# Kernel optimization log

Measured on AMD Instinct MI355X. Metric: run time of the kernel, lower is better.

The kernel has to match this reference:

```python
import jax, jax.numpy as jnp
import numpy as np

STRIDES = (8, 16, 32)
FMP = ((160, 160), (80, 80), (40, 40))
NUM_CLASSES = 80
TOPK = 1000
CONF_THRESH = 0.05
NMS_THRESH = 0.6
IMG_MAX = 1280.0
CLASS_OFFSET = 8192.0  # > any box coordinate, separates classes for batched NMS


def setup_inputs() -> dict:
    key = jax.random.key(0)
    ks = jax.random.split(key, 32)
    C = 256
    inp = {}
    for l, (h, w) in enumerate(FMP):
        inp[f'feat{l}'] = jax.random.normal(ks[l], (1, C, h, w), dtype=jnp.float32)
        inp[f'Wobj{l}'] = jax.random.normal(ks[3 + 6 * l + 0], (1, C), dtype=jnp.float32) * 0.05
        inp[f'bobj{l}'] = jnp.zeros((1,), dtype=jnp.float32)
        inp[f'Wcls{l}'] = jax.random.normal(ks[3 + 6 * l + 2], (NUM_CLASSES, C), dtype=jnp.float32) * 0.05
        inp[f'bcls{l}'] = jnp.zeros((NUM_CLASSES,), dtype=jnp.float32)
        inp[f'Wreg{l}'] = jax.random.normal(ks[3 + 6 * l + 4], (4, C), dtype=jnp.float32) * 0.05
        inp[f'breg{l}'] = jnp.zeros((4,), dtype=jnp.float32)
    return inp


def _level(feat, Wo, bo, Wc, bc, Wr, br, stride):
    x = feat[0]  # [C,H,W]
    H, W = x.shape[1], x.shape[2]
    def conv1x1(Wm, bv):
        # 1x1 conv == channel GEMM; output [H*W, O]
        return (jnp.einsum('oc,chw->hwo', Wm, x) + bv).reshape(H * W, -1)
    obj = conv1x1(Wo, bo)              # [M,1]
    cls = conv1x1(Wc, bc)              # [M,C]
    reg = jnp.exp(conv1x1(Wr, br)) * stride  # [M,4] (l,t,r,b)
    prob = jax.nn.sigmoid(obj) * jax.nn.sigmoid(cls)
    scores = prob.max(axis=-1)
    labels = prob.argmax(axis=-1)
    ay, ax = jnp.meshgrid(jnp.arange(H), jnp.arange(W), indexing='ij')
    anchors = (jnp.stack([ax, ay], axis=-1).astype(jnp.float32).reshape(-1, 2) + 0.5) * stride
    k = min(TOPK, H * W)
    scores, idx = jax.lax.top_k(scores, k)
    labels = labels[idx]
    reg = reg[idx]
    anchors = anchors[idx]
    boxes = jnp.concatenate([anchors - reg[:, :2], anchors + reg[:, 2:]], axis=-1)
    return scores, labels, boxes


def _batched_nms(boxes, scores, labels):
    N = boxes.shape[0]
    valid = scores >= CONF_THRESH
    # class-offset trick: per-class NMS == single NMS on disjoint offset boxes
    ob = boxes + labels.astype(boxes.dtype)[:, None] * CLASS_OFFSET
    order = jnp.argsort(-scores)
    b = ob[order]
    v = valid[order]
    x1, y1, x2, y2 = b[:, 0], b[:, 1], b[:, 2], b[:, 3]
    areas = (x2 - x1) * (y2 - y1)
    xx1 = jnp.maximum(x1[:, None], x1[None, :])
    yy1 = jnp.maximum(y1[:, None], y1[None, :])
    xx2 = jnp.minimum(x2[:, None], x2[None, :])
    yy2 = jnp.minimum(y2[:, None], y2[None, :])
    w = jnp.maximum(1e-10, xx2 - xx1)
    h = jnp.maximum(1e-10, yy2 - yy1)
    inter = w * h
    iou = inter / (areas[:, None] + areas[None, :] - inter + 1e-14)
    idxs = jnp.arange(N)
    def body(i, keep):
        sup = keep[i] & (iou[i] > NMS_THRESH) & (idxs > i)
        return keep & ~sup
    keep_sorted = jax.lax.fori_loop(0, N, body, v)
    keep = jnp.zeros(N, dtype=bool).at[order].set(keep_sorted)
    return keep


def reference(feat0, feat1, feat2,
              Wobj0, bobj0, Wcls0, bcls0, Wreg0, breg0,
              Wobj1, bobj1, Wcls1, bcls1, Wreg1, breg1,
              Wobj2, bobj2, Wcls2, bcls2, Wreg2, breg2):
    feats = (feat0, feat1, feat2)
    params = ((Wobj0, bobj0, Wcls0, bcls0, Wreg0, breg0),
              (Wobj1, bobj1, Wcls1, bcls1, Wreg1, breg1),
              (Wobj2, bobj2, Wcls2, bcls2, Wreg2, breg2))
    ss, ll, bb = [], [], []
    for l in range(3):
        s, lab, box = _level(feats[l], *params[l], STRIDES[l])
        ss.append(s); ll.append(lab); bb.append(box)
    scores = jnp.concatenate(ss)
    labels = jnp.concatenate(ll)
    boxes = jnp.concatenate(bb)
    keep = _batched_nms(boxes, scores, labels)
    bboxes = jnp.clip(boxes / IMG_MAX, 0.0, 1.0)
    return bboxes, scores, labels.astype(jnp.int32), keep
```

## Files before the change

kernel.cpp:

```cpp
#include <hip/hip_runtime.h>
#include <math.h>

#define NTOT   33600
#define NSEL   3000
#define CAND_CAP 8192
#define NWORDS 47
#define NROWS_PAD 3008
#define FCAP 4
#define NGRP 525
#define WPER 21760

struct P21 {
  const float* feat[3];
  const float* Wobj[3];
  const float* bobj[3];
  const float* Wcls[3];
  const float* bcls[3];
  const float* Wreg[3];
  const float* breg[3];
};

__device__ __forceinline__ void level_of_block(int b, int t, int& l, int& p, int& g,
                                               int& HW, int& Wd, double& stride) {
  if (b < 100)      { l = 0; p = b * 256 + t;         g = p;          HW = 25600; Wd = 160; stride = 8.0;  }
  else if (b < 125) { l = 1; p = (b - 100) * 256 + t; g = 25600 + p;  HW = 6400;  Wd = 80;  stride = 16.0; }
  else              { l = 2; p = (b - 125) * 256 + t; g = 32000 + p;  HW = 1600;  Wd = 40;  stride = 32.0; }
}

__device__ __forceinline__ void level_of_group(int grp, int lane, int& l, int& p, int& g,
                                               int& HW, int& Wd, double& stride) {
  if (grp < 400)      { l = 0; p = grp * 64 + lane;         g = p;         HW = 25600; Wd = 160; stride = 8.0;  }
  else if (grp < 500) { l = 1; p = (grp - 400) * 64 + lane; g = 25600 + p; HW = 6400;  Wd = 80;  stride = 16.0; }
  else                { l = 2; p = (grp - 500) * 64 + lane; g = 32000 + p; HW = 1600;  Wd = 40;  stride = 32.0; }
}

__device__ __forceinline__ double sigmoid_d(double x) { return 1.0 / (1.0 + exp(-x)); }

__device__ __forceinline__ unsigned long long shfl64(unsigned long long v, int src) {
  unsigned lo = (unsigned)__shfl((int)(unsigned)(v & 0xFFFFFFFFull), src, 64);
  unsigned hi = (unsigned)__shfl((int)(unsigned)(v >> 32), src, 64);
  return (((unsigned long long)hi) << 32) | (unsigned long long)lo;
}

__global__ __launch_bounds__(256) void k_wconv(P21 P, double* __restrict__ W64) {
  int id = blockIdx.x * 256 + threadIdx.x;
  if (id >= 3 * WPER) return;
  int l = id / WPER, r = id - l * WPER;
  const float* src;
  if (r < 256)        src = P.Wobj[l] + r;
  else if (r < 1280)  src = P.Wreg[l] + (r - 256);
  else                src = P.Wcls[l] + (r - 1280);
  W64[id] = (double)(*src);
}

__global__ __launch_bounds__(256) void k_conv_chunk(P21 P, const double* __restrict__ W64,
    double* __restrict__ obj_t, double* __restrict__ reg_t,
    double* __restrict__ cmax, int* __restrict__ clab) {
  int l, p, g, HW, Wd; double stride;
  level_of_block(blockIdx.x, threadIdx.x, l, p, g, HW, Wd, stride);
  if (p >= HW) return;
  const int ch = blockIdx.y;
  const float* __restrict__ fp = P.feat[l] + p;
  const double* __restrict__ Wl = W64 + l * WPER;

  if (ch == 0) {
    const double* __restrict__ Wo = Wl;
    const double* __restrict__ Wr = Wl + 256;
    double accO = (double)P.bobj[l][0];
    double accR[4];
#pragma unroll
    for (int j = 0; j < 4; j++) accR[j] = (double)P.breg[l][j];
    for (int c = 0; c < 256; c += 8) {
      double xc[8];
#pragma unroll
      for (int u = 0; u < 8; u++) xc[u] = (double)fp[(c + u) * HW];
#pragma unroll
      for (int u = 0; u < 8; u++) {
        accO = fma(Wo[c + u], xc[u], accO);
#pragma unroll
        for (int j = 0; j < 4; j++)
          accR[j] = fma(Wr[j * 256 + c + u], xc[u], accR[j]);
      }
    }
    obj_t[g] = accO;
#pragma unroll
    for (int j = 0; j < 4; j++) reg_t[4 * g + j] = accR[j];
  } else {
    const int base = (ch - 1) * 8;
    const double* __restrict__ Wc = Wl + 1280 + base * 256;
    const float* __restrict__ bcls = P.bcls[l];
    double a[8];
#pragma unroll
    for (int j = 0; j < 8; j++) a[j] = (double)bcls[base + j];
    for (int c = 0; c < 256; c += 8) {
      double xc[8];
#pragma unroll
      for (int u = 0; u < 8; u++) xc[u] = (double)fp[(c + u) * HW];
#pragma unroll
      for (int u = 0; u < 8; u++) {
#pragma unroll
        for (int j = 0; j < 8; j++)
          a[j] = fma(Wc[j * 256 + c + u], xc[u], a[j]);
      }
    }
    double maxv = a[0]; int lab = base;
#pragma unroll
    for (int j = 1; j < 8; j++) if (a[j] > maxv) { maxv = a[j]; lab = base + j; }
    cmax[(ch - 1) * NTOT + g] = maxv;
    clab[(ch - 1) * NTOT + g] = lab;
  }
}

__global__ __launch_bounds__(64) void k_combine(
    const double* __restrict__ obj_t, const double* __restrict__ reg_t,
    const double* __restrict__ cmax, const int* __restrict__ clab,
    double* __restrict__ score_d, int* __restrict__ label_d,
    double* __restrict__ box_d, unsigned* __restrict__ hist) {
  int l, p, g, HW, Wd; double stride;
  level_of_group(blockIdx.x, threadIdx.x, l, p, g, HW, Wd, stride);

  double maxv = cmax[g]; int lab = clab[g];
#pragma unroll
  for (int k = 1; k < 10; k++) {
    double v = cmax[k * NTOT + g];
    int lb = clab[k * NTOT + g];
    if (v > maxv) { maxv = v; lab = lb; }
  }
  double score = sigmoid_d(obj_t[g]) * sigmoid_d(maxv);
  int h = p / Wd, w = p - h * Wd;
  double ax = ((double)w + 0.5) * stride;
  double ay = ((double)h + 0.5) * stride;
  double e0 = exp(reg_t[4 * g + 0]) * stride;
  double e1 = exp(reg_t[4 * g + 1]) * stride;
  double e2 = exp(reg_t[4 * g + 2]) * stride;
  double e3 = exp(reg_t[4 * g + 3]) * stride;

  score_d[g] = score;
  label_d[g] = lab;
  box_d[4 * g + 0] = ax - e0;
  box_d[4 * g + 1] = ay - e1;
  box_d[4 * g + 2] = ax + e2;
  box_d[4 * g + 3] = ay + e3;

  unsigned key = __float_as_uint((float)score);
  atomicAdd(&hist[l * 65536 + (key >> 16)], 1u);
}

__global__ __launch_bounds__(256) void k_scan_a(const unsigned* __restrict__ hist,
                                                unsigned* __restrict__ csG) {
  const int lane = threadIdx.x & 63;
  const int row = blockIdx.x * 4 + (threadIdx.x >> 6);
  const uint4* hp = (const uint4*)(hist + row * 256);
  uint4 v = hp[lane];
  unsigned s = v.x + v.y + v.z + v.w;
#pragma unroll
  for (int off = 32; off > 0; off >>= 1) s += (unsigned)__shfl_down((int)s, off, 64);
  if (lane == 0) csG[row] = s;
}

__global__ __launch_bounds__(256) void k_scan_b(const unsigned* __restrict__ hist,
                                                const unsigned* __restrict__ csG,
                                                unsigned* __restrict__ cutB) {
  int l = blockIdx.x;
  __shared__ unsigned cs[256];
  __shared__ unsigned hb[256];
  __shared__ int s_chunk;
  __shared__ unsigned s_acc;
  int t = threadIdx.x;
  cs[t] = csG[l * 256 + t];
  __syncthreads();
  if (t == 0) {
    unsigned acc = 0; int chunk = 0;
    for (int tt = 255; tt >= 0; tt--) {
      if (acc + cs[tt] >= 1000u) { chunk = tt; break; }
      acc += cs[tt];
    }
    s_chunk = chunk; s_acc = acc;
  }
  __syncthreads();
  int chunk = s_chunk;
  hb[t] = hist[l * 65536 + chunk * 256 + t];
  __syncthreads();
  if (t == 0) {
    unsigned acc = s_acc;
    unsigned B = (unsigned)(chunk * 256);
    for (int b = 255; b >= 0; b--) {
      unsigned c = hb[b];
      if (acc + c >= 1000u) { B = (unsigned)(chunk * 256 + b); break; }
      acc += c;
    }
    cutB[l] = B;
  }
}

__global__ __launch_bounds__(64) void k_compact(const double* __restrict__ score_d,
    const unsigned* __restrict__ cutB, unsigned* __restrict__ cnt,
    double* __restrict__ cand_s, int* __restrict__ cand_g) {
  int l, p, g, HW, Wd; double stride;
  level_of_group(blockIdx.x, threadIdx.x, l, p, g, HW, Wd, stride);
  double sc = score_d[g];
  unsigned key = __float_as_uint((float)sc);
  if ((key >> 16) >= cutB[l]) {
    unsigned pos = atomicAdd(&cnt[l], 1u);
    if (pos < CAND_CAP) {
      cand_s[l * CAND_CAP + pos] = sc;
      cand_g[l * CAND_CAP + pos] = g;
    }
  }
}

__global__ __launch_bounds__(256) void k_rank(const double* __restrict__ cand_s,
    const int* __restrict__ cand_g, const unsigned* __restrict__ cnt,
    const int* __restrict__ label_d, const double* __restrict__ box_d,
    double* __restrict__ sel_s, int* __restrict__ sel_lab, double* __restrict__ sel_box) {
  const int l = blockIdx.y;
  const int M = (int)min(cnt[l], (unsigned)CAND_CAP);
  if (blockIdx.x * 4 >= M) return;
  const int q = blockIdx.x * 4 + (threadIdx.x >> 6);
  const int lane = threadIdx.x & 63;
  const bool active = (q < M);

  double s = 0.0; int g = 0;
  if (active) { s = cand_s[l * CAND_CAP + q]; g = cand_g[l * CAND_CAP + q]; }

  int r = 0;
  if (active) {
    for (int j = lane; j < M; j += 64) {
      double sj = cand_s[l * CAND_CAP + j];
      int gj = cand_g[l * CAND_CAP + j];
      r += (sj > s) || (sj == s && gj < g);
    }
  }
#pragma unroll
  for (int off = 32; off > 0; off >>= 1) r += __shfl_down(r, off, 64);

  if (active && lane == 0 && r < 1000) {
    int o = l * 1000 + r;
    sel_s[o] = s;
    sel_lab[o] = label_d[g];
    sel_box[4 * o + 0] = box_d[4 * g + 0];
    sel_box[4 * o + 1] = box_d[4 * g + 1];
    sel_box[4 * o + 2] = box_d[4 * g + 2];
    sel_box[4 * o + 3] = box_d[4 * g + 3];
  }
}

__global__ __launch_bounds__(256) void k_order(const double* __restrict__ sel_s,
                                               int* __restrict__ sortIdx) {
  const int i = blockIdx.x;
  const int t = threadIdx.x;
  const double s = sel_s[i];
  int r = 0;
  for (int j = t; j < NSEL; j += 256) {
    double sj = sel_s[j];
    r += (sj > s) || (sj == s && j < i);
  }
#pragma unroll
  for (int off = 32; off > 0; off >>= 1) r += __shfl_down(r, off, 64);
  __shared__ int wsum[4];
  if ((t & 63) == 0) wsum[t >> 6] = r;
  __syncthreads();
  if (t == 0) sortIdx[wsum[0] + wsum[1] + wsum[2] + wsum[3]] = i;
}

__global__ __launch_bounds__(256) void k_build(const double* __restrict__ sel_s,
    const int* __restrict__ sel_lab, const double* __restrict__ sel_box,
    const int* __restrict__ sortIdx, double* __restrict__ sbox, int* __restrict__ svalid) {
  int r = blockIdx.x * 256 + threadIdx.x;
  if (r >= NSEL) return;
  int i = sortIdx[r];
  double off = (double)sel_lab[i] * 8192.0;
  sbox[4 * r + 0] = sel_box[4 * i + 0] + off;
  sbox[4 * r + 1] = sel_box[4 * i + 1] + off;
  sbox[4 * r + 2] = sel_box[4 * i + 2] + off;
  sbox[4 * r + 3] = sel_box[4 * i + 3] + off;
  svalid[r] = (sel_s[i] >= 0.05) ? 1 : 0;
}

__global__ __launch_bounds__(256) void k_mask(const double* __restrict__ sbox,
    unsigned long long* __restrict__ denseG, unsigned long long* __restrict__ diagG,
    unsigned short* __restrict__ entG, unsigned short* __restrict__ cntG) {
  __shared__ unsigned long long wordS[48];
  __shared__ unsigned short entS[FCAP];
  __shared__ int cntS;
  const int i = blockIdx.x;
  const int t = threadIdx.x, lane = t & 63, wk = t >> 6;
  if (t == 0) cntS = 0;
  const double x1 = sbox[4 * i + 0], y1 = sbox[4 * i + 1];
  const double x2 = sbox[4 * i + 2], y2 = sbox[4 * i + 3];
  const double ar = (x2 - x1) * (y2 - y1);
  const int iw = i >> 6;
  __syncthreads();
  for (int w = wk; w < NWORDS; w += 4) {
    int j = w * 64 + lane;
    bool c = false;
    if (j < NSEL && j > i) {
      double bx1 = sbox[4 * j + 0], by1 = sbox[4 * j + 1];
      double bx2 = sbox[4 * j + 2], by2 = sbox[4 * j + 3];
      double arj = (bx2 - bx1) * (by2 - by1);
      double xx1 = fmax(x1, bx1), yy1 = fmax(y1, by1);
      double xx2 = fmin(x2, bx2), yy2 = fmin(y2, by2);
      double ww = fmax(1e-10, xx2 - xx1);
      double hh = fmax(1e-10, yy2 - yy1);
      double inter = ww * hh;
      double iou = inter / (ar + arj - inter + 1e-14);
      c = iou > 0.6;
    }
    unsigned long long word = __ballot(c);
    if (lane == 0) {
      wordS[w] = word;
      if (w > iw && word) {
        unsigned long long tt = word;
        while (tt) {
          int b = __builtin_ctzll(tt); tt &= tt - 1;
          int slot = atomicAdd(&cntS, 1);
          if (slot < FCAP) entS[slot] = (unsigned short)(w * 64 + b);
        }
      }
    }
  }
  __syncthreads();
  if (t < NWORDS) denseG[(size_t)i * 48 + t] = wordS[t];
  if (t == 0) {
    diagG[i] = wordS[iw];
    int c = cntS;
    cntG[i] = (unsigned short)c;
    int cs = c < FCAP ? c : FCAP;
    for (int k = 0; k < cs; k++) entG[i * FCAP + k] = entS[k];
    for (int k = cs; k < FCAP; k++) entG[i * FCAP + k] = 0;
  }
}

__global__ __launch_bounds__(256) void k_nms_scan(
    const unsigned long long* __restrict__ denseG, const unsigned long long* __restrict__ diagG,
    const unsigned short* __restrict__ entG, const unsigned short* __restrict__ cntG,
    const int* __restrict__ svalid, const int* __restrict__ sortIdx,
    int* __restrict__ keepOrig) {
  __shared__ unsigned long long diagL[NROWS_PAD];
  __shared__ unsigned short entL[NROWS_PAD * FCAP];
  __shared__ unsigned short cntL[NROWS_PAD];
  __shared__ unsigned long long validL[48];
  __shared__ unsigned long long hasWL[48];
  const int t = threadIdx.x;
  const int lane = t & 63;

  for (int k = t; k < NSEL; k += 256) diagL[k] = diagG[k];
  for (int k = NSEL + t; k < NROWS_PAD; k += 256) diagL[k] = 0ull;
  uint2* e2 = (uint2*)entL; const uint2* eg2 = (const uint2*)entG;
  for (int k = t; k < NSEL; k += 256) e2[k] = eg2[k];
  for (int k = NSEL + t; k < NROWS_PAD; k += 256) { uint2 z; z.x = 0; z.y = 0; e2[k] = z; }
  unsigned* c2 = (unsigned*)cntL; const unsigned* cg2 = (const unsigned*)cntG;
  for (int k = t; k < NSEL / 2; k += 256) c2[k] = cg2[k];
  for (int k = NSEL / 2 + t; k < NROWS_PAD / 2; k += 256) c2[k] = 0;
  for (int i0 = t; i0 < NROWS_PAD; i0 += 256) {
    bool f = (i0 < NSEL) && (svalid[i0] != 0);
    unsigned long long b = __ballot(f);
    if ((t & 63) == 0) validL[i0 >> 6] = b;
  }
  __syncthreads();
  if (t >= 64) return;

  for (int w = 0; w < NWORDS; w++) {
    int i = w * 64 + lane;
    bool f = (diagL[i] != 0ull) || (cntL[i] != 0);
    unsigned long long b = __ballot(f);
    if (lane == 0) hasWL[w] = b;
  }

  unsigned long long rem = 0ull;
  unsigned long long keep = 0ull;
  for (int w = 0; w < NWORDS; w++) {
    unsigned long long vw = validL[w];
    unsigned long long remw = shfl64(rem, w);
    unsigned long long win = vw & ~remw;
    unsigned long long work = hasWL[w];
    while (work) {
      int d = __builtin_ctzll(work); work &= work - 1;
      if ((win >> d) & 1ull) {
        int i = w * 64 + d;
        win &= ~diagL[i];
        int c = cntL[i];
        if (c > FCAP) {
          unsigned long long rowj = (lane < NWORDS) ? denseG[(size_t)i * 48 + lane] : 0ull;
          rem |= rowj;
        } else {
          for (int k = 0; k < c; k++) {
            int j = entL[i * FCAP + k];
            if ((j >> 6) == lane) rem |= 1ull << (j & 63);
          }
        }
      }
    }
    if (lane == w) keep = win;
  }
  if (lane < NWORDS) {
    for (int b = 0; b < 64; b++) {
      int j = lane * 64 + b;
      if (j < NSEL) keepOrig[sortIdx[j]] = (int)((keep >> b) & 1ull);
    }
  }
}

__global__ __launch_bounds__(256) void k_out(const double* __restrict__ sel_s,
    const int* __restrict__ sel_lab, const double* __restrict__ sel_box,
    const int* __restrict__ keepOrig, float* __restrict__ out) {
  int i = blockIdx.x * 256 + threadIdx.x;
  if (i >= NSEL) return;
#pragma unroll
  for (int c = 0; c < 4; c++) {
    double v = sel_box[4 * i + c] / 1280.0;
    v = fmin(fmax(v, 0.0), 1.0);
    out[4 * i + c] = (float)v;
  }
  out[12000 + i] = (float)sel_s[i];
  out[15000 + i] = (float)sel_lab[i];
  out[18000 + i] = keepOrig[i] ? 1.0f : 0.0f;
}

extern "C" void kernel_launch(void* const* d_in, const int* in_sizes, int n_in,
                              void* d_out, int out_size, void* d_ws, size_t ws_size,
                              hipStream_t stream) {
  P21 P;
  for (int l = 0; l < 3; l++) {
    P.feat[l] = (const float*)d_in[7 * l + 0];
    P.Wobj[l] = (const float*)d_in[7 * l + 1];
    P.bobj[l] = (const float*)d_in[7 * l + 2];
    P.Wcls[l] = (const float*)d_in[7 * l + 3];
    P.bcls[l] = (const float*)d_in[7 * l + 4];
    P.Wreg[l] = (const float*)d_in[7 * l + 5];
    P.breg[l] = (const float*)d_in[7 * l + 6];
  }

  char* ws = (char*)d_ws;
  size_t off = 0;
  auto alloc = [&](size_t bytes) -> char* {
    char* p = ws + off;
    off += (bytes + 15) & ~(size_t)15;
    return p;
  };
  double* score_d  = (double*)alloc((size_t)NTOT * 8);
  double* box_d    = (double*)alloc((size_t)NTOT * 4 * 8);
  int*    label_d  = (int*)   alloc((size_t)NTOT * 4);
  double* obj_t    = (double*)alloc((size_t)NTOT * 8);
  double* reg_t    = (double*)alloc((size_t)NTOT * 4 * 8);
  double* cmax     = (double*)alloc((size_t)10 * NTOT * 8);
  int*    clab     = (int*)   alloc((size_t)10 * NTOT * 4);
  double* W64      = (double*)alloc((size_t)3 * WPER * 8);
  double* sel_s    = (double*)alloc((size_t)NSEL * 8);
  double* sel_box  = (double*)alloc((size_t)NSEL * 4 * 8);
  int*    sel_lab  = (int*)   alloc((size_t)NSEL * 4);
  int*    sortIdx  = (int*)   alloc((size_t)NSEL * 4);
  double* sbox     = (double*)alloc((size_t)NSEL * 4 * 8);
  int*    svalid   = (int*)   alloc((size_t)NSEL * 4);
  int*    keepOrig = (int*)   alloc((size_t)NSEL * 4);
  double* cand_s   = (double*)alloc((size_t)3 * CAND_CAP * 8);
  int*    cand_g   = (int*)   alloc((size_t)3 * CAND_CAP * 4);
  unsigned long long* denseG = (unsigned long long*)alloc((size_t)NSEL * 48 * 8);
  unsigned long long* diagG  = (unsigned long long*)alloc((size_t)NSEL * 8);
  unsigned short*     entG   = (unsigned short*)alloc((size_t)NSEL * FCAP * 2);
  unsigned short*     cntG   = (unsigned short*)alloc((size_t)NSEL * 2);
  unsigned* hist   = (unsigned*)alloc((size_t)3 * 65536 * 4);
  unsigned* cnt    = (unsigned*)alloc(16);
  unsigned* cutB   = (unsigned*)alloc(16);
  unsigned* csG    = (unsigned*)alloc((size_t)768 * 4);

  hipMemsetAsync(hist, 0, (size_t)3 * 65536 * 4 + 16, stream);

  k_wconv   <<<(3 * WPER + 255) / 256, 256, 0, stream>>>(P, W64);
  dim3 cgrid(132, 11, 1);
  k_conv_chunk<<<cgrid, 256, 0, stream>>>(P, W64, obj_t, reg_t, cmax, clab);
  k_combine <<<NGRP, 64, 0, stream>>>(obj_t, reg_t, cmax, clab, score_d, label_d, box_d, hist);
  k_scan_a  <<<192, 256, 0, stream>>>(hist, csG);
  k_scan_b  <<<3, 256, 0, stream>>>(hist, csG, cutB);
  k_compact <<<NGRP, 64, 0, stream>>>(score_d, cutB, cnt, cand_s, cand_g);
  dim3 rgrid(CAND_CAP / 4, 3, 1);
  k_rank    <<<rgrid, 256, 0, stream>>>(cand_s, cand_g, cnt, label_d, box_d,
                                        sel_s, sel_lab, sel_box);
  k_order   <<<NSEL, 256, 0, stream>>>(sel_s, sortIdx);
  k_build   <<<(NSEL + 255) / 256, 256, 0, stream>>>(sel_s, sel_lab, sel_box, sortIdx, sbox, svalid);
  k_mask    <<<NSEL, 256, 0, stream>>>(sbox, denseG, diagG, entG, cntG);
  k_nms_scan<<<1, 256, 0, stream>>>(denseG, diagG, entG, cntG, svalid, sortIdx, keepOrig);
  k_out     <<<(NSEL + 255) / 256, 256, 0, stream>>>(sel_s, sel_lab, sel_box, keepOrig, (float*)d_out);
}
```

Measured before the change: 269.1 us.

## Split class conv into finer slices and tile NMS mask over 64x64 blocks

The class 1x1-conv now runs 16 slices of 5 classes each with 128-thread blocks, replacing 10 slices of 8 with 256 threads. That gives more blocks and fewer live accumulators per thread. The IoU mask kernel moves from one block per row to a 2D grid of 64-row by 64-column tiles. Row boxes are staged in shared memory, and tiles below the diagonal just write zeros. Per-row far-hit lists are now built with global atomics on a zeroed int counter array, which adds atomic traffic and leaves unused entry slots unzeroed.

New measurement: 307.0 us. 1.14x slower.

```diff
diff --git a/kernel.cpp b/kernel.cpp
--- a/kernel.cpp
+++ b/kernel.cpp
@@ -9,6 +9,8 @@
 #define FCAP 4
 #define NGRP 525
 #define WPER 21760
+#define NCH 17
+#define NSLC 16
 
 struct P21 {
   const float* feat[3];
@@ -20,11 +22,11 @@
   const float* breg[3];
 };
 
-__device__ __forceinline__ void level_of_block(int b, int t, int& l, int& p, int& g,
-                                               int& HW, int& Wd, double& stride) {
-  if (b < 100)      { l = 0; p = b * 256 + t;         g = p;          HW = 25600; Wd = 160; stride = 8.0;  }
-  else if (b < 125) { l = 1; p = (b - 100) * 256 + t; g = 25600 + p;  HW = 6400;  Wd = 80;  stride = 16.0; }
-  else              { l = 2; p = (b - 125) * 256 + t; g = 32000 + p;  HW = 1600;  Wd = 40;  stride = 32.0; }
+__device__ __forceinline__ void level_of_block128(int b, int t, int& l, int& p, int& g,
+                                                  int& HW, int& Wd, double& stride) {
+  if (b < 200)      { l = 0; p = b * 128 + t;         g = p;          HW = 25600; Wd = 160; stride = 8.0;  }
+  else if (b < 250) { l = 1; p = (b - 200) * 128 + t; g = 25600 + p;  HW = 6400;  Wd = 80;  stride = 16.0; }
+  else              { l = 2; p = (b - 250) * 128 + t; g = 32000 + p;  HW = 1600;  Wd = 40;  stride = 32.0; }
 }
 
 __device__ __forceinline__ void level_of_group(int grp, int lane, int& l, int& p, int& g,
@@ -53,11 +55,11 @@
   W64[id] = (double)(*src);
 }
 
-__global__ __launch_bounds__(256) void k_conv_chunk(P21 P, const double* __restrict__ W64,
+__global__ __launch_bounds__(128) void k_conv_chunk(P21 P, const double* __restrict__ W64,
     double* __restrict__ obj_t, double* __restrict__ reg_t,
     double* __restrict__ cmax, int* __restrict__ clab) {
   int l, p, g, HW, Wd; double stride;
-  level_of_block(blockIdx.x, threadIdx.x, l, p, g, HW, Wd, stride);
+  level_of_block128(blockIdx.x, threadIdx.x, l, p, g, HW, Wd, stride);
   if (p >= HW) return;
   const int ch = blockIdx.y;
   const float* __restrict__ fp = P.feat[l] + p;
@@ -86,12 +88,12 @@
 #pragma unroll
     for (int j = 0; j < 4; j++) reg_t[4 * g + j] = accR[j];
   } else {
-    const int base = (ch - 1) * 8;
+    const int base = (ch - 1) * 5;
     const double* __restrict__ Wc = Wl + 1280 + base * 256;
     const float* __restrict__ bcls = P.bcls[l];
-    double a[8];
-#pragma unroll
-    for (int j = 0; j < 8; j++) a[j] = (double)bcls[base + j];
+    double a[5];
+#pragma unroll
+    for (int j = 0; j < 5; j++) a[j] = (double)bcls[base + j];
     for (int c = 0; c < 256; c += 8) {
       double xc[8];
 #pragma unroll
@@ -99,13 +101,13 @@
 #pragma unroll
       for (int u = 0; u < 8; u++) {
 #pragma unroll
-        for (int j = 0; j < 8; j++)
+        for (int j = 0; j < 5; j++)
           a[j] = fma(Wc[j * 256 + c + u], xc[u], a[j]);
       }
     }
     double maxv = a[0]; int lab = base;
 #pragma unroll
-    for (int j = 1; j < 8; j++) if (a[j] > maxv) { maxv = a[j]; lab = base + j; }
+    for (int j = 1; j < 5; j++) if (a[j] > maxv) { maxv = a[j]; lab = base + j; }
     cmax[(ch - 1) * NTOT + g] = maxv;
     clab[(ch - 1) * NTOT + g] = lab;
   }
@@ -121,7 +123,7 @@
 
   double maxv = cmax[g]; int lab = clab[g];
 #pragma unroll
-  for (int k = 1; k < 10; k++) {
+  for (int k = 1; k < NSLC; k++) {
     double v = cmax[k * NTOT + g];
     int lb = clab[k * NTOT + g];
     if (v > maxv) { maxv = v; lab = lb; }
@@ -279,25 +281,40 @@
 
 __global__ __launch_bounds__(256) void k_mask(const double* __restrict__ sbox,
     unsigned long long* __restrict__ denseG, unsigned long long* __restrict__ diagG,
-    unsigned short* __restrict__ entG, unsigned short* __restrict__ cntG) {
-  __shared__ unsigned long long wordS[48];
-  __shared__ unsigned short entS[FCAP];
-  __shared__ int cntS;
-  const int i = blockIdx.x;
+    unsigned short* __restrict__ entG, int* __restrict__ cntGi) {
+  const int w = blockIdx.x;
+  const int rc = blockIdx.y;
   const int t = threadIdx.x, lane = t & 63, wk = t >> 6;
-  if (t == 0) cntS = 0;
-  const double x1 = sbox[4 * i + 0], y1 = sbox[4 * i + 1];
-  const double x2 = sbox[4 * i + 2], y2 = sbox[4 * i + 3];
-  const double ar = (x2 - x1) * (y2 - y1);
-  const int iw = i >> 6;
-  __syncthreads();
-  for (int w = wk; w < NWORDS; w += 4) {
-    int j = w * 64 + lane;
+  const int rbase = rc * 64;
+  if (w < rc) {
+    int i = rbase + t;
+    if (t < 64 && i < NSEL) denseG[(size_t)i * 48 + w] = 0ull;
+    return;
+  }
+  __shared__ double rbox[256];
+  {
+    int idx = rbase * 4 + t;
+    rbox[t] = (idx < NSEL * 4) ? sbox[idx] : 0.0;
+  }
+  const int j = w * 64 + lane;
+  const bool jok = (j < NSEL);
+  double bx1 = 0, by1 = 0, bx2 = 0, by2 = 0, arj = 0;
+  if (jok) {
+    bx1 = sbox[4 * j + 0]; by1 = sbox[4 * j + 1];
+    bx2 = sbox[4 * j + 2]; by2 = sbox[4 * j + 3];
+    arj = (bx2 - bx1) * (by2 - by1);
+  }
+  __syncthreads();
+#pragma unroll
+  for (int rr = 0; rr < 16; rr++) {
+    const int ro = wk * 16 + rr;
+    const int i = rbase + ro;
+    if (i >= NSEL) break;
+    double x1 = rbox[ro * 4 + 0], y1 = rbox[ro * 4 + 1];
+    double x2 = rbox[ro * 4 + 2], y2 = rbox[ro * 4 + 3];
+    double ar = (x2 - x1) * (y2 - y1);
     bool c = false;
-    if (j < NSEL && j > i) {
-      double bx1 = sbox[4 * j + 0], by1 = sbox[4 * j + 1];
-      double bx2 = sbox[4 * j + 2], by2 = sbox[4 * j + 3];
-      double arj = (bx2 - bx1) * (by2 - by1);
+    if (jok && j > i) {
       double xx1 = fmax(x1, bx1), yy1 = fmax(y1, by1);
       double xx2 = fmin(x2, bx2), yy2 = fmin(y2, by2);
       double ww = fmax(1e-10, xx2 - xx1);
@@ -308,32 +325,23 @@
     }
     unsigned long long word = __ballot(c);
     if (lane == 0) {
-      wordS[w] = word;
-      if (w > iw && word) {
+      denseG[(size_t)i * 48 + w] = word;
+      if (w == rc) diagG[i] = word;
+      else if (word) {
         unsigned long long tt = word;
         while (tt) {
           int b = __builtin_ctzll(tt); tt &= tt - 1;
-          int slot = atomicAdd(&cntS, 1);
-          if (slot < FCAP) entS[slot] = (unsigned short)(w * 64 + b);
+          int slot = atomicAdd(&cntGi[i], 1);
+          if (slot < FCAP) entG[i * FCAP + slot] = (unsigned short)(w * 64 + b);
         }
       }
     }
   }
-  __syncthreads();
-  if (t < NWORDS) denseG[(size_t)i * 48 + t] = wordS[t];
-  if (t == 0) {
-    diagG[i] = wordS[iw];
-    int c = cntS;
-    cntG[i] = (unsigned short)c;
-    int cs = c < FCAP ? c : FCAP;
-    for (int k = 0; k < cs; k++) entG[i * FCAP + k] = entS[k];
-    for (int k = cs; k < FCAP; k++) entG[i * FCAP + k] = 0;
-  }
 }
 
 __global__ __launch_bounds__(256) void k_nms_scan(
     const unsigned long long* __restrict__ denseG, const unsigned long long* __restrict__ diagG,
-    const unsigned short* __restrict__ entG, const unsigned short* __restrict__ cntG,
+    const unsigned short* __restrict__ entG, const int* __restrict__ cntGi,
     const int* __restrict__ svalid, const int* __restrict__ sortIdx,
     int* __restrict__ keepOrig) {
   __shared__ unsigned long long diagL[NROWS_PAD];
@@ -349,9 +357,8 @@
   uint2* e2 = (uint2*)entL; const uint2* eg2 = (const uint2*)entG;
   for (int k = t; k < NSEL; k += 256) e2[k] = eg2[k];
   for (int k = NSEL + t; k < NROWS_PAD; k += 256) { uint2 z; z.x = 0; z.y = 0; e2[k] = z; }
-  unsigned* c2 = (unsigned*)cntL; const unsigned* cg2 = (const unsigned*)cntG;
-  for (int k = t; k < NSEL / 2; k += 256) c2[k] = cg2[k];
-  for (int k = NSEL / 2 + t; k < NROWS_PAD / 2; k += 256) c2[k] = 0;
+  for (int k = t; k < NSEL; k += 256) cntL[k] = (unsigned short)cntGi[k];
+  for (int k = NSEL + t; k < NROWS_PAD; k += 256) cntL[k] = 0;
   for (int i0 = t; i0 < NROWS_PAD; i0 += 256) {
     bool f = (i0 < NSEL) && (svalid[i0] != 0);
     unsigned long long b = __ballot(f);
@@ -443,8 +450,8 @@
   int*    label_d  = (int*)   alloc((size_t)NTOT * 4);
   double* obj_t    = (double*)alloc((size_t)NTOT * 8);
   double* reg_t    = (double*)alloc((size_t)NTOT * 4 * 8);
-  double* cmax     = (double*)alloc((size_t)10 * NTOT * 8);
-  int*    clab     = (int*)   alloc((size_t)10 * NTOT * 4);
+  double* cmax     = (double*)alloc((size_t)NSLC * NTOT * 8);
+  int*    clab     = (int*)   alloc((size_t)NSLC * NTOT * 4);
   double* W64      = (double*)alloc((size_t)3 * WPER * 8);
   double* sel_s    = (double*)alloc((size_t)NSEL * 8);
   double* sel_box  = (double*)alloc((size_t)NSEL * 4 * 8);
@@ -458,17 +465,17 @@
   unsigned long long* denseG = (unsigned long long*)alloc((size_t)NSEL * 48 * 8);
   unsigned long long* diagG  = (unsigned long long*)alloc((size_t)NSEL * 8);
   unsigned short*     entG   = (unsigned short*)alloc((size_t)NSEL * FCAP * 2);
-  unsigned short*     cntG   = (unsigned short*)alloc((size_t)NSEL * 2);
   unsigned* hist   = (unsigned*)alloc((size_t)3 * 65536 * 4);
   unsigned* cnt    = (unsigned*)alloc(16);
+  int*      cntGi  = (int*)   alloc((size_t)NSEL * 4);
   unsigned* cutB   = (unsigned*)alloc(16);
   unsigned* csG    = (unsigned*)alloc((size_t)768 * 4);
 
-  hipMemsetAsync(hist, 0, (size_t)3 * 65536 * 4 + 16, stream);
+  hipMemsetAsync(hist, 0, (size_t)3 * 65536 * 4 + 16 + (size_t)NSEL * 4, stream);
 
   k_wconv   <<<(3 * WPER + 255) / 256, 256, 0, stream>>>(P, W64);
-  dim3 cgrid(132, 11, 1);
-  k_conv_chunk<<<cgrid, 256, 0, stream>>>(P, W64, obj_t, reg_t, cmax, clab);
+  dim3 cgrid(263, NCH, 1);
+  k_conv_chunk<<<cgrid, 128, 0, stream>>>(P, W64, obj_t, reg_t, cmax, clab);
   k_combine <<<NGRP, 64, 0, stream>>>(obj_t, reg_t, cmax, clab, score_d, label_d, box_d, hist);
   k_scan_a  <<<192, 256, 0, stream>>>(hist, csG);
   k_scan_b  <<<3, 256, 0, stream>>>(hist, csG, cutB);
@@ -478,7 +485,8 @@
                                         sel_s, sel_lab, sel_box);
   k_order   <<<NSEL, 256, 0, stream>>>(sel_s, sortIdx);
   k_build   <<<(NSEL + 255) / 256, 256, 0, stream>>>(sel_s, sel_lab, sel_box, sortIdx, sbox, svalid);
-  k_mask    <<<NSEL, 256, 0, stream>>>(sbox, denseG, diagG, entG, cntG);
-  k_nms_scan<<<1, 256, 0, stream>>>(denseG, diagG, entG, cntG, svalid, sortIdx, keepOrig);
+  dim3 mgrid(NWORDS, NWORDS, 1);
+  k_mask    <<<mgrid, 256, 0, stream>>>(sbox, denseG, diagG, entG, cntGi);
+  k_nms_scan<<<1, 256, 0, stream>>>(denseG, diagG, entG, cntGi, svalid, sortIdx, keepOrig);
   k_out     <<<(NSEL + 255) / 256, 256, 0, stream>>>(sel_s, sel_lab, sel_box, keepOrig, (float*)d_out);
 }
```
